# Kernel tuning notes

Measured on AMD Instinct MI355X. Metric: run time of the kernel, lower is better.

The kernel has to match this reference:

```python
import jax, jax.numpy as jnp
import numpy as np

NH, NKV, HD, H = 32, 8, 128, 4096
G = NH // NKV  # GQA group size = 4
EPS = 1e-5
SCALE = HD ** -0.5


def rms_norm(x, w, eps=EPS):
    # per-head RMSNorm over last dim, computed in fp32
    xf = x.astype(jnp.float32)
    var = jnp.mean(xf * xf, axis=-1, keepdims=True)
    return (w * (xf * jax.lax.rsqrt(var + eps)).astype(x.dtype))


def setup_inputs() -> dict:
    key = jax.random.key(0)
    ks = jax.random.split(key, 4)
    B, SQ, SKV = 4, 1024, 1601
    return {
        "hidden_states": jax.random.normal(ks[0], (B, SQ, H), jnp.float32),
        "cross_attention_states": jax.random.normal(ks[1], (B, SKV, H), jnp.float32),
        "wqkv": jax.random.normal(ks[2], ((NH + 2 * NKV) * HD, H), jnp.float32) * 0.02,
        "wo": jax.random.normal(ks[3], (NH * HD, H), jnp.float32) * 0.02,
        "q_norm_weight": jnp.ones((HD,), jnp.float32),
        "k_norm_weight": jnp.ones((HD,), jnp.float32),
    }


def reference(hidden_states, cross_attention_states, wqkv, wo, q_norm_weight, k_norm_weight):
    B, SQ, _ = hidden_states.shape
    SKV = cross_attention_states.shape[1]
    q_sz, kv_sz = NH * HD, NKV * HD

    # fused QKV projection on decoder tokens -> keep only q
    qkv_dec = jnp.einsum('bsh,oh->bso', hidden_states, wqkv)
    q = qkv_dec[..., :q_sz]
    # fused QKV projection on encoder tokens -> keep only k, v
    qkv_enc = jnp.einsum('bsh,oh->bso', cross_attention_states, wqkv)
    k = qkv_enc[..., q_sz:q_sz + kv_sz]
    v = qkv_enc[..., q_sz + kv_sz:]

    q = rms_norm(q.reshape(B, SQ, NH, HD), q_norm_weight)      # [B,SQ,NH,HD]
    k = rms_norm(k.reshape(B, SKV, NKV, HD), k_norm_weight)    # [B,SKV,NKV,HD]
    v = v.reshape(B, SKV, NKV, HD)

    # GQA: group query heads per kv head
    qg = q.reshape(B, SQ, NKV, G, HD)
    scores = jnp.einsum('bqkgd,bskd->bkgqs', qg, k) * SCALE    # [B,NKV,G,SQ,SKV]
    probs = jax.nn.softmax(scores, axis=-1)
    out = jnp.einsum('bkgqs,bskd->bqkgd', probs, v)            # [B,SQ,NKV,G,HD]
    out = out.reshape(B, SQ, NH * HD)
    return jnp.einsum('bso,ho->bsh', out, wo.T.T) if False else jnp.einsum('bsf,hf->bsh', out, wo)
```

## Files before the change

### kernel.cpp

```cpp
#include <hip/hip_runtime.h>
#include <cstdint>
#include <math.h>

typedef _Float16 f16;
typedef __attribute__((ext_vector_type(4))) _Float16 f16x4;
typedef __attribute__((ext_vector_type(8))) _Float16 f16x8;
typedef __attribute__((ext_vector_type(4))) float f32x4;

__device__ inline void gload_lds16(const void* g, void* l) {
  auto gp = reinterpret_cast<const __attribute__((address_space(1))) uint32_t*>(
      reinterpret_cast<uintptr_t>(g));
  auto lp = reinterpret_cast<__attribute__((address_space(3))) uint32_t*>(
      reinterpret_cast<uintptr_t>(l));
  __builtin_amdgcn_global_load_lds(gp, lp, 16 , 0, 0);
}

__global__ __launch_bounds__(256) void cvtzero_kernel(const float* __restrict__ s0, f16* __restrict__ d0,
                                                      const float* __restrict__ s1, f16* __restrict__ d1,
                                                      const float* __restrict__ s2, f16* __restrict__ d2,
                                                      float4* __restrict__ z) {
  int idx = blockIdx.x * blockDim.x + threadIdx.x;
  int stride = gridDim.x * blockDim.x;
  for (int i = idx; i < 18747392; i += stride) {
    const float* src; f16* dst; int k;
    if (i < 4194304) { src = s0; dst = d0; k = i; }
    else if (i < 10752000) { src = s1; dst = d1; k = i - 4194304; }
    else if (i < 17043456) { src = s2; dst = d2; k = i - 10752000; }
    else { float4 zr = {0.f, 0.f, 0.f, 0.f}; z[i - 17043456] = zr; continue; }
    float4 v = reinterpret_cast<const float4*>(src)[k];
    f16x4 h;
    h.x = (f16)v.x; h.y = (f16)v.y; h.z = (f16)v.z; h.w = (f16)v.w;
    reinterpret_cast<f16x4*>(dst)[k] = h;
  }
}

__global__ __launch_bounds__(256) void cvt_kernel(const float* __restrict__ src,
                                                  f16* __restrict__ dst, int n4) {
  int idx = blockIdx.x * blockDim.x + threadIdx.x;
  int stride = gridDim.x * blockDim.x;
  for (int i = idx; i < n4; i += stride) {
    float4 v = reinterpret_cast<const float4*>(src)[i];
    f16x4 h;
    h.x = (f16)v.x; h.y = (f16)v.y; h.z = (f16)v.z; h.w = (f16)v.w;
    reinterpret_cast<f16x4*>(dst)[i] = h;
  }
}

template <bool MB, int EPI>
__global__ __launch_bounds__(512, 2) void gemm256(const f16* __restrict__ A,
                                                  const f16* __restrict__ Bw,
                                                  float* __restrict__ C,
                                                  f16* __restrict__ Ch,
                                                  const float* __restrict__ wvec,
                                                  f16* __restrict__ Vtf,
                                                  int M, int N, int K) {
  __shared__ f16 As[2][256][64];
  __shared__ f16 Bs[2][256][64];
  const int tid = threadIdx.x;
  const int l = tid & 63, w = tid >> 6;
  const int lq = l & 15, lk = l >> 4;
  const int wm = w >> 2, wn = w & 3;
  const int nwg = gridDim.x * gridDim.y;
  const int p = blockIdx.y * gridDim.x + blockIdx.x;
  const int L = (p & 7) * (nwg >> 3) + (p >> 3);
  const int bx = L % gridDim.x, by = L / gridDim.x;
  const int brow = by * 256, bcol = bx * 256;
  const int KT = K >> 6;

  const int srow8 = w * 8 + (l >> 3);
  const int scol  = ((l & 7) ^ (l >> 3)) * 8;
  const int swz   = (lq & 7) << 4;

  f32x4 acc[8][4];
  f32x4 zf = {0.f, 0.f, 0.f, 0.f};
#pragma unroll
  for (int m = 0; m < 8; ++m)
#pragma unroll
    for (int n = 0; n < 4; ++n) acc[m][n] = zf;

  auto stageA = [&](int kt, int buf, int i) {
    int ra = brow + i * 64 + srow8;
    if (MB) ra = (ra < M) ? ra : (M - 1);
    gload_lds16(A + (size_t)ra * K + kt * 64 + scol,
                (char*)(&As[buf][0][0]) + i * 8192 + w * 1024);
  };
  auto stageB = [&](int kt, int buf, int i) {
    int rb = bcol + i * 64 + srow8;
    gload_lds16(Bw + (size_t)rb * K + kt * 64 + scol,
                (char*)(&Bs[buf][0][0]) + i * 8192 + w * 1024);
  };
  auto ldA = [&](int buf, int m, int kk) -> f16x8 {
    int r = wm * 128 + m * 16 + lq;
    return *reinterpret_cast<const f16x8*>(
        (char*)(&As[buf][0][0]) + r * 128 + ((kk * 64 + lk * 16) ^ swz));
  };
  auto ldB = [&](int buf, int n, int kk) -> f16x8 {
    int r = wn * 64 + n * 16 + lq;
    return *reinterpret_cast<const f16x8*>(
        (char*)(&Bs[buf][0][0]) + r * 128 + ((kk * 64 + lk * 16) ^ swz));
  };

#pragma unroll
  for (int i = 0; i < 4; ++i) stageA(0, 0, i);
#pragma unroll
  for (int i = 0; i < 4; ++i) stageB(0, 0, i);

  f16x8 avA[4][2], avB[4][2], bvA[2][2], bvB[2][2];
  for (int t = 0; t < KT; ++t) {
    const int buf = t & 1, nbuf = buf ^ 1;
    const bool pf = (t + 1 < KT);

    if (pf) {
      stageA(t + 1, nbuf, 0); stageA(t + 1, nbuf, 1);
      asm volatile("s_waitcnt vmcnt(2)" ::: "memory");
    } else {
      asm volatile("s_waitcnt vmcnt(0)" ::: "memory");
    }
    __builtin_amdgcn_s_barrier();

#pragma unroll
    for (int mm = 0; mm < 4; ++mm)
#pragma unroll
      for (int kk = 0; kk < 2; ++kk) avA[mm][kk] = ldA(buf, mm, kk);
#pragma unroll
    for (int nn = 0; nn < 2; ++nn)
#pragma unroll
      for (int kk = 0; kk < 2; ++kk) bvA[nn][kk] = ldB(buf, nn, kk);
    __builtin_amdgcn_s_setprio(1);
#pragma unroll
    for (int mm = 0; mm < 4; ++mm)
#pragma unroll
      for (int nn = 0; nn < 2; ++nn)
#pragma unroll
        for (int kk = 0; kk < 2; ++kk)
          acc[mm][nn] = __builtin_amdgcn_mfma_f32_16x16x32_f16(avA[mm][kk], bvA[nn][kk], acc[mm][nn], 0, 0, 0);
    __builtin_amdgcn_s_setprio(0);
#pragma unroll
    for (int mm = 0; mm < 4; ++mm)
#pragma unroll
      for (int kk = 0; kk < 2; ++kk) avB[mm][kk] = ldA(buf, 4 + mm, kk);
    if (pf) { stageA(t + 1, nbuf, 2); stageA(t + 1, nbuf, 3); }
    asm volatile("" ::: "memory");
    __builtin_amdgcn_s_barrier();

    __builtin_amdgcn_s_setprio(1);
#pragma unroll
    for (int mm = 0; mm < 4; ++mm)
#pragma unroll
      for (int nn = 0; nn < 2; ++nn)
#pragma unroll
        for (int kk = 0; kk < 2; ++kk)
          acc[4 + mm][nn] = __builtin_amdgcn_mfma_f32_16x16x32_f16(avB[mm][kk], bvA[nn][kk], acc[4 + mm][nn], 0, 0, 0);
    __builtin_amdgcn_s_setprio(0);
#pragma unroll
    for (int nn = 0; nn < 2; ++nn)
#pragma unroll
      for (int kk = 0; kk < 2; ++kk) bvB[nn][kk] = ldB(buf, 2 + nn, kk);
    if (pf) { stageB(t + 1, nbuf, 0); stageB(t + 1, nbuf, 1); }
    asm volatile("" ::: "memory");
    __builtin_amdgcn_s_barrier();

    __builtin_amdgcn_s_setprio(1);
#pragma unroll
    for (int mm = 0; mm < 4; ++mm)
#pragma unroll
      for (int nn = 0; nn < 2; ++nn)
#pragma unroll
        for (int kk = 0; kk < 2; ++kk)
          acc[4 + mm][2 + nn] = __builtin_amdgcn_mfma_f32_16x16x32_f16(avB[mm][kk], bvB[nn][kk], acc[4 + mm][2 + nn], 0, 0, 0);
    __builtin_amdgcn_s_setprio(0);
#pragma unroll
    for (int mm = 0; mm < 4; ++mm)
#pragma unroll
      for (int kk = 0; kk < 2; ++kk) avA[mm][kk] = ldA(buf, mm, kk);
    if (pf) { stageB(t + 1, nbuf, 2); stageB(t + 1, nbuf, 3); }
    asm volatile("" ::: "memory");
    __builtin_amdgcn_s_barrier();

    __builtin_amdgcn_s_setprio(1);
#pragma unroll
    for (int mm = 0; mm < 4; ++mm)
#pragma unroll
      for (int nn = 0; nn < 2; ++nn)
#pragma unroll
        for (int kk = 0; kk < 2; ++kk)
          acc[mm][2 + nn] = __builtin_amdgcn_mfma_f32_16x16x32_f16(avA[mm][kk], bvB[nn][kk], acc[mm][2 + nn], 0, 0, 0);
    __builtin_amdgcn_s_setprio(0);
  }

  if (EPI == 0) {
#pragma unroll
    for (int m = 0; m < 8; ++m) {
#pragma unroll
      for (int j = 0; j < 4; ++j) {
        int row = brow + wm * 128 + m * 16 + lk * 4 + j;
        if (MB && row >= M) continue;
        float* dst = C + (size_t)row * N + bcol + wn * 64 + lq;
#pragma unroll
        for (int n = 0; n < 4; ++n) dst[n * 16] = acc[m][n][j];
      }
    }
  } else if (EPI == 1) {
    __shared__ float ssq[256][4];
#pragma unroll
    for (int m = 0; m < 8; ++m)
#pragma unroll
      for (int j = 0; j < 4; ++j) {
        int lr = wm * 128 + m * 16 + lk * 4 + j;
        float pp = 0.f;
#pragma unroll
        for (int n = 0; n < 4; ++n) pp += acc[m][n][j] * acc[m][n][j];
        pp += __shfl_xor(pp, 1);
        pp += __shfl_xor(pp, 2);
        pp += __shfl_xor(pp, 4);
        pp += __shfl_xor(pp, 8);
        if (lq == 0) ssq[lr][wn] = pp;
      }
    asm volatile("" ::: "memory");
    __builtin_amdgcn_s_barrier();
    const int hh = wn >> 1;
    float wv[4];
#pragma unroll
    for (int n = 0; n < 4; ++n) wv[n] = wvec[(wn * 64 + n * 16 + lq) & 127];
#pragma unroll
    for (int m = 0; m < 8; ++m)
#pragma unroll
      for (int j = 0; j < 4; ++j) {
        int lr = wm * 128 + m * 16 + lk * 4 + j;
        float ss = ssq[lr][hh * 2] + ssq[lr][hh * 2 + 1];
        float rs = rsqrtf(ss * (1.0f / 128.0f) + 1e-5f) *
                   (0.08838834764831845f * 1.4426950408889634f);
        f16* dst = Ch + (size_t)(brow + lr) * N + bcol + wn * 64 + lq;
#pragma unroll
        for (int n = 0; n < 4; ++n) dst[n * 16] = (f16)(acc[m][n][j] * rs * wv[n]);
      }
  } else {
    const bool isK = (bcol < 1024);
    __shared__ float ssq[256][4];
    if (isK) {
#pragma unroll
      for (int m = 0; m < 8; ++m)
#pragma unroll
        for (int j = 0; j < 4; ++j) {
          int lr = wm * 128 + m * 16 + lk * 4 + j;
          float pp = 0.f;
#pragma unroll
          for (int n = 0; n < 4; ++n) pp += acc[m][n][j] * acc[m][n][j];
          pp += __shfl_xor(pp, 1);
          pp += __shfl_xor(pp, 2);
          pp += __shfl_xor(pp, 4);
          pp += __shfl_xor(pp, 8);
          if (lq == 0) ssq[lr][wn] = pp;
        }
      asm volatile("" ::: "memory");
      __builtin_amdgcn_s_barrier();
    }
    const int hh = wn >> 1;
    float wv[4];
    if (isK) {
#pragma unroll
      for (int n = 0; n < 4; ++n) wv[n] = wvec[(wn * 64 + n * 16 + lq) & 127];
    }
#pragma unroll
    for (int m = 0; m < 8; ++m) {
#pragma unroll
      for (int j = 0; j < 4; ++j) {
        int lr = wm * 128 + m * 16 + lk * 4 + j;
        int r = brow + lr;
        if (r >= M) continue;
        unsigned bb = (unsigned)r / 1601u;
        unsigned s = (unsigned)r - bb * 1601u;
        if (isK) {
          float ss = ssq[lr][hh * 2] + ssq[lr][hh * 2 + 1];
          float rs = rsqrtf(ss * (1.0f / 128.0f) + 1e-5f);
#pragma unroll
          for (int n = 0; n < 4; ++n) {
            int col = wn * 64 + n * 16 + lq;
            int kvh = (bcol + col) >> 7;
            int d = col & 127;
            Ch[((size_t)(bb * 8 + kvh) * 1664 + s) * 128 + d] =
                (f16)(acc[m][n][j] * rs * wv[n]);
          }
        } else {
#pragma unroll
          for (int n = 0; n < 4; ++n) {
            int col = bcol - 1024 + wn * 64 + n * 16 + lq;
            int kvh = col >> 7;
            int d = col & 127;
            Vtf[((size_t)(bb * 8 + kvh) * 128 + d) * 1664 + s] = (f16)acc[m][n][j];
          }
        }
      }
    }
  }
}

__global__ __launch_bounds__(512, 4) void attn_kernel(const f16* __restrict__ Qf,
                                                      const f16* __restrict__ Kf,
                                                      const f16* __restrict__ Vtf,
                                                      f16* __restrict__ Oa) {
  __shared__ f16 Ksm[2][64][128];
  __shared__ f16 Vsm[2][128][64];
  __shared__ f16 Psm[8][16][64];
  const int p = blockIdx.x;
  const int L = (p & 7) * 128 + (p >> 3);
  const int qt = L & 7, h = (L >> 3) & 31, b = L >> 8;
  const int kvh = h >> 2;
  const int tid = threadIdx.x;
  const int l = tid & 63, w = tid >> 6;
  const int lq = l & 15, lk = l >> 4;

  f16x8 qreg[4];
  const f16* Qbase = Qf + ((size_t)(b * 1024 + qt * 128 + w * 16)) * 4096 + h * 128;
#pragma unroll
  for (int ks = 0; ks < 4; ++ks)
    qreg[ks] = *reinterpret_cast<const f16x8*>(
        Qbase + (size_t)lq * 4096 + ks * 32 + lk * 8);

  const f16* Kb = Kf + (size_t)(b * 8 + kvh) * (1664 * 128);
  const f16* Vb = Vtf + (size_t)(b * 8 + kvh) * (128 * 1664);

  f32x4 o[8];
  f32x4 zf = {0.f, 0.f, 0.f, 0.f};
  f32x4 neg8 = {-8.f, -8.f, -8.f, -8.f};
#pragma unroll
  for (int dn = 0; dn < 8; ++dn) o[dn] = zf;
  float lrow[4];
#pragma unroll
  for (int j = 0; j < 4; ++j) lrow[j] = 0.f;

  char* Pw = (char*)(&Psm[w][0][0]);
  const int swzR = (lq & 7) << 4;

  auto stageK = [&](int t, int buf) {
#pragma unroll
    for (int i = 0; i < 2; ++i) {
      int row = w * 8 + i * 4 + lk;
      int cb = (lq * 16) ^ ((row & 7) << 4);
      gload_lds16(Kb + (size_t)(t * 64 + row) * 128 + (cb >> 1),
                  (char*)(&Ksm[buf][0][0]) + w * 2048 + i * 1024);
    }
  };
  auto stageV = [&](int t, int buf) {
#pragma unroll
    for (int i = 0; i < 2; ++i) {
      int r = w * 16 + i * 8 + (l >> 3);
      int cb = ((l & 7) * 16) ^ ((r & 7) << 4);
      gload_lds16(Vb + (size_t)r * 1664 + t * 64 + (cb >> 1),
                  (char*)(&Vsm[buf][0][0]) + w * 2048 + i * 1024);
    }
  };

  stageK(0, 0);
  stageV(0, 0);
  int cur = 0;
  for (int t = 0; t < 26; ++t) {
    if (t < 25) {
      stageK(t + 1, cur ^ 1);
      stageV(t + 1, cur ^ 1);
      asm volatile("s_waitcnt vmcnt(4)" ::: "memory");
    } else {
      asm volatile("s_waitcnt vmcnt(0)" ::: "memory");
    }
    __builtin_amdgcn_s_barrier();

    f32x4 s[4];
#pragma unroll
    for (int kn = 0; kn < 4; ++kn) s[kn] = neg8;
    __builtin_amdgcn_s_setprio(1);
#pragma unroll
    for (int ks = 0; ks < 4; ++ks) {
      f16x8 bf[4];
#pragma unroll
      for (int kn = 0; kn < 4; ++kn)
        bf[kn] = *reinterpret_cast<const f16x8*>(
            (char*)(&Ksm[cur][0][0]) + (kn * 16 + lq) * 256 + ((ks * 64 + lk * 16) ^ swzR));
#pragma unroll
      for (int kn = 0; kn < 4; ++kn)
        s[kn] = __builtin_amdgcn_mfma_f32_16x16x32_f16(qreg[ks], bf[kn], s[kn], 0, 0, 0);
    }
    __builtin_amdgcn_s_setprio(0);

    if (t == 25) {
#pragma unroll
      for (int kn = 0; kn < 4; ++kn) {
        bool valid = (kn * 16 + lq) < 1;
#pragma unroll
        for (int j = 0; j < 4; ++j) s[kn][j] = valid ? s[kn][j] : -1e30f;
      }
    }

#pragma unroll
    for (int j = 0; j < 4; ++j) {
      float rsum = 0.f;
#pragma unroll
      for (int kn = 0; kn < 4; ++kn) {
        float pv = exp2f(s[kn][j]);
        s[kn][j] = pv;
        rsum += pv;
      }
      lrow[j] += rsum;
      int prow = lk * 4 + j;
      int swzW = (prow & 7) << 4;
#pragma unroll
      for (int kn = 0; kn < 4; ++kn)
        *reinterpret_cast<f16*>(Pw + prow * 128 + (((kn * 16 + lq) * 2) ^ swzW)) =
            (f16)s[kn][j];
    }

    __builtin_amdgcn_s_setprio(1);
#pragma unroll
    for (int c = 0; c < 2; ++c) {
      f16x8 pa = *reinterpret_cast<const f16x8*>(
          Pw + lq * 128 + ((c * 64 + lk * 16) ^ swzR));
      f16x8 vb[8];
#pragma unroll
      for (int dn = 0; dn < 8; ++dn)
        vb[dn] = *reinterpret_cast<const f16x8*>(
            (char*)(&Vsm[cur][0][0]) + (dn * 16 + lq) * 128 + ((c * 64 + lk * 16) ^ swzR));
#pragma unroll
      for (int dn = 0; dn < 8; ++dn)
        o[dn] = __builtin_amdgcn_mfma_f32_16x16x32_f16(pa, vb[dn], o[dn], 0, 0, 0);
    }
    __builtin_amdgcn_s_setprio(0);
    __builtin_amdgcn_s_barrier();
    cur ^= 1;
  }

#pragma unroll
  for (int j = 0; j < 4; ++j) {
    float fl = lrow[j];
    fl += __shfl_xor(fl, 1);
    fl += __shfl_xor(fl, 2);
    fl += __shfl_xor(fl, 4);
    fl += __shfl_xor(fl, 8);
    float il = 1.0f / fl;
    int token = b * 1024 + qt * 128 + w * 16 + lk * 4 + j;
    f16* dst = Oa + (size_t)token * 4096 + h * 128;
#pragma unroll
    for (int dn = 0; dn < 8; ++dn) dst[dn * 16 + lq] = (f16)(o[dn][j] * il);
  }
}

extern "C" void kernel_launch(void* const* d_in, const int* in_sizes, int n_in,
                              void* d_out, int out_size, void* d_ws, size_t ws_size,
                              hipStream_t stream) {
  const float* hidden = (const float*)d_in[0];
  const float* cross  = (const float*)d_in[1];
  const float* wqkv   = (const float*)d_in[2];
  const float* wo     = (const float*)d_in[3];
  const float* qw     = (const float*)d_in[4];
  const float* kw     = (const float*)d_in[5];

  char* ws = (char*)d_ws;
  f16* hidden_h = (f16*)(ws + 0);
  f16* attn_h   = hidden_h;
  f16* wqkv_h = (f16*)(ws + 33554432);
  f16* cross_h = (f16*)(ws + 83886080);
  f16* wo_h    = (f16*)(ws + 83886080);
  f16* k_h  = (f16*)(ws + 136347648);
  f16* vt_h = (f16*)(ws + 136347648 + 13631488);
  f16* q_h = (f16*)d_out;

  cvtzero_kernel<<<2048, 256, 0, stream>>>(hidden, hidden_h, cross, cross_h,
                                           wqkv, wqkv_h, (float4*)(ws + 136347648));
  gemm256<true, 2><<<dim3(8, 26), 512, 0, stream>>>(
      cross_h, wqkv_h + (size_t)4096 * 4096, nullptr, k_h, kw, vt_h, 6404, 2048, 4096);
  cvt_kernel<<<2048, 256, 0, stream>>>(wo, wo_h, 16777216 / 4);
  gemm256<false, 1><<<dim3(16, 16), 512, 0, stream>>>(
      hidden_h, wqkv_h, nullptr, q_h, qw, nullptr, 4096, 4096, 4096);
  attn_kernel<<<1024, 512, 0, stream>>>(q_h, k_h, vt_h, attn_h);
  gemm256<false, 0><<<dim3(16, 16), 512, 0, stream>>>(
      attn_h, wo_h, (float*)d_out, nullptr, nullptr, nullptr, 4096, 4096, 4096);
}
```

Baseline: 613.5 us.

## Give each attention wave two query sub-tiles to reuse K/V LDS fragments

```diff
diff --git a/kernel.cpp b/kernel.cpp
--- a/kernel.cpp
+++ b/kernel.cpp
@@ -295,13 +295,13 @@
   }
 }
 
-__global__ __launch_bounds__(512, 4) void attn_kernel(const f16* __restrict__ Qf,
+__global__ __launch_bounds__(256, 2) void attn_kernel(const f16* __restrict__ Qf,
                                                       const f16* __restrict__ Kf,
                                                       const f16* __restrict__ Vtf,
                                                       f16* __restrict__ Oa) {
   __shared__ f16 Ksm[2][64][128];
   __shared__ f16 Vsm[2][128][64];
-  __shared__ f16 Psm[8][16][64];
+  __shared__ f16 Psm[4][32][64];
   const int p = blockIdx.x;
   const int L = (p & 7) * 128 + (p >> 3);
   const int qt = L & 7, h = (L >> 3) & 31, b = L >> 8;
@@ -310,44 +310,50 @@
   const int l = tid & 63, w = tid >> 6;
   const int lq = l & 15, lk = l >> 4;
 
-  f16x8 qreg[4];
-  const f16* Qbase = Qf + ((size_t)(b * 1024 + qt * 128 + w * 16)) * 4096 + h * 128;
-#pragma unroll
-  for (int ks = 0; ks < 4; ++ks)
-    qreg[ks] = *reinterpret_cast<const f16x8*>(
-        Qbase + (size_t)lq * 4096 + ks * 32 + lk * 8);
+  f16x8 qreg[2][4];
+  const f16* Qbase = Qf + ((size_t)(b * 1024 + qt * 128 + w * 32)) * 4096 + h * 128;
+#pragma unroll
+  for (int qm = 0; qm < 2; ++qm)
+#pragma unroll
+    for (int ks = 0; ks < 4; ++ks)
+      qreg[qm][ks] = *reinterpret_cast<const f16x8*>(
+          Qbase + (size_t)(qm * 16 + lq) * 4096 + ks * 32 + lk * 8);
 
   const f16* Kb = Kf + (size_t)(b * 8 + kvh) * (1664 * 128);
   const f16* Vb = Vtf + (size_t)(b * 8 + kvh) * (128 * 1664);
 
-  f32x4 o[8];
+  f32x4 o[2][8];
   f32x4 zf = {0.f, 0.f, 0.f, 0.f};
   f32x4 neg8 = {-8.f, -8.f, -8.f, -8.f};
 #pragma unroll
-  for (int dn = 0; dn < 8; ++dn) o[dn] = zf;
-  float lrow[4];
-#pragma unroll
-  for (int j = 0; j < 4; ++j) lrow[j] = 0.f;
+  for (int qm = 0; qm < 2; ++qm)
+#pragma unroll
+    for (int dn = 0; dn < 8; ++dn) o[qm][dn] = zf;
+  float lrow[2][4];
+#pragma unroll
+  for (int qm = 0; qm < 2; ++qm)
+#pragma unroll
+    for (int j = 0; j < 4; ++j) lrow[qm][j] = 0.f;
 
   char* Pw = (char*)(&Psm[w][0][0]);
   const int swzR = (lq & 7) << 4;
 
   auto stageK = [&](int t, int buf) {
 #pragma unroll
-    for (int i = 0; i < 2; ++i) {
-      int row = w * 8 + i * 4 + lk;
+    for (int i = 0; i < 4; ++i) {
+      int row = w * 16 + i * 4 + lk;
       int cb = (lq * 16) ^ ((row & 7) << 4);
       gload_lds16(Kb + (size_t)(t * 64 + row) * 128 + (cb >> 1),
-                  (char*)(&Ksm[buf][0][0]) + w * 2048 + i * 1024);
+                  (char*)(&Ksm[buf][0][0]) + w * 4096 + i * 1024);
     }
   };
   auto stageV = [&](int t, int buf) {
 #pragma unroll
-    for (int i = 0; i < 2; ++i) {
-      int r = w * 16 + i * 8 + (l >> 3);
+    for (int i = 0; i < 4; ++i) {
+      int r = w * 32 + i * 8 + (l >> 3);
       int cb = ((l & 7) * 16) ^ ((r & 7) << 4);
       gload_lds16(Vb + (size_t)r * 1664 + t * 64 + (cb >> 1),
-                  (char*)(&Vsm[buf][0][0]) + w * 2048 + i * 1024);
+                  (char*)(&Vsm[buf][0][0]) + w * 4096 + i * 1024);
     }
   };
 
@@ -358,15 +364,17 @@
     if (t < 25) {
       stageK(t + 1, cur ^ 1);
       stageV(t + 1, cur ^ 1);
-      asm volatile("s_waitcnt vmcnt(4)" ::: "memory");
+      asm volatile("s_waitcnt vmcnt(8)" ::: "memory");
     } else {
       asm volatile("s_waitcnt vmcnt(0)" ::: "memory");
     }
     __builtin_amdgcn_s_barrier();
 
-    f32x4 s[4];
-#pragma unroll
-    for (int kn = 0; kn < 4; ++kn) s[kn] = neg8;
+    f32x4 s[2][4];
+#pragma unroll
+    for (int qm = 0; qm < 2; ++qm)
+#pragma unroll
+      for (int kn = 0; kn < 4; ++kn) s[qm][kn] = neg8;
     __builtin_amdgcn_s_setprio(1);
 #pragma unroll
     for (int ks = 0; ks < 4; ++ks) {
@@ -376,8 +384,10 @@
         bf[kn] = *reinterpret_cast<const f16x8*>(
             (char*)(&Ksm[cur][0][0]) + (kn * 16 + lq) * 256 + ((ks * 64 + lk * 16) ^ swzR));
 #pragma unroll
-      for (int kn = 0; kn < 4; ++kn)
-        s[kn] = __builtin_amdgcn_mfma_f32_16x16x32_f16(qreg[ks], bf[kn], s[kn], 0, 0, 0);
+      for (int qm = 0; qm < 2; ++qm)
+#pragma unroll
+        for (int kn = 0; kn < 4; ++kn)
+          s[qm][kn] = __builtin_amdgcn_mfma_f32_16x16x32_f16(qreg[qm][ks], bf[kn], s[qm][kn], 0, 0, 0);
     }
     __builtin_amdgcn_s_setprio(0);
 
@@ -386,41 +396,53 @@
       for (int kn = 0; kn < 4; ++kn) {
         bool valid = (kn * 16 + lq) < 1;
 #pragma unroll
-        for (int j = 0; j < 4; ++j) s[kn][j] = valid ? s[kn][j] : -1e30f;
-      }
-    }
-
-#pragma unroll
-    for (int j = 0; j < 4; ++j) {
-      float rsum = 0.f;
-#pragma unroll
-      for (int kn = 0; kn < 4; ++kn) {
-        float pv = exp2f(s[kn][j]);
-        s[kn][j] = pv;
-        rsum += pv;
-      }
-      lrow[j] += rsum;
-      int prow = lk * 4 + j;
-      int swzW = (prow & 7) << 4;
-#pragma unroll
-      for (int kn = 0; kn < 4; ++kn)
-        *reinterpret_cast<f16*>(Pw + prow * 128 + (((kn * 16 + lq) * 2) ^ swzW)) =
-            (f16)s[kn][j];
+        for (int qm = 0; qm < 2; ++qm)
+#pragma unroll
+          for (int j = 0; j < 4; ++j) s[qm][kn][j] = valid ? s[qm][kn][j] : -1e30f;
+      }
+    }
+
+#pragma unroll
+    for (int qm = 0; qm < 2; ++qm) {
+#pragma unroll
+      for (int j = 0; j < 4; ++j) {
+        float rsum = 0.f;
+#pragma unroll
+        for (int kn = 0; kn < 4; ++kn) {
+          float pv = exp2f(s[qm][kn][j]);
+          s[qm][kn][j] = pv;
+          rsum += pv;
+        }
+        lrow[qm][j] += rsum;
+        int prow = qm * 16 + lk * 4 + j;
+        int swzW = lk << 5;
+#pragma unroll
+        for (int kn = 0; kn < 4; ++kn)
+          *reinterpret_cast<f16*>(Pw + prow * 128 + (((kn * 16 + lq) * 2) ^ swzW)) =
+              (f16)s[qm][kn][j];
+      }
     }
 
     __builtin_amdgcn_s_setprio(1);
 #pragma unroll
     for (int c = 0; c < 2; ++c) {
-      f16x8 pa = *reinterpret_cast<const f16x8*>(
-          Pw + lq * 128 + ((c * 64 + lk * 16) ^ swzR));
+      f16x8 pa[2];
+#pragma unroll
+      for (int qm = 0; qm < 2; ++qm) {
+        int prow = qm * 16 + lq;
+        pa[qm] = *reinterpret_cast<const f16x8*>(
+            Pw + prow * 128 + ((c * 64 + lk * 16) ^ (((lq >> 2) & 3) << 5)));
+      }
       f16x8 vb[8];
 #pragma unroll
       for (int dn = 0; dn < 8; ++dn)
         vb[dn] = *reinterpret_cast<const f16x8*>(
             (char*)(&Vsm[cur][0][0]) + (dn * 16 + lq) * 128 + ((c * 64 + lk * 16) ^ swzR));
 #pragma unroll
-      for (int dn = 0; dn < 8; ++dn)
-        o[dn] = __builtin_amdgcn_mfma_f32_16x16x32_f16(pa, vb[dn], o[dn], 0, 0, 0);
+      for (int qm = 0; qm < 2; ++qm)
+#pragma unroll
+        for (int dn = 0; dn < 8; ++dn)
+          o[qm][dn] = __builtin_amdgcn_mfma_f32_16x16x32_f16(pa[qm], vb[dn], o[qm][dn], 0, 0, 0);
     }
     __builtin_amdgcn_s_setprio(0);
     __builtin_amdgcn_s_barrier();
@@ -428,17 +450,20 @@
   }
 
 #pragma unroll
-  for (int j = 0; j < 4; ++j) {
-    float fl = lrow[j];
-    fl += __shfl_xor(fl, 1);
-    fl += __shfl_xor(fl, 2);
-    fl += __shfl_xor(fl, 4);
-    fl += __shfl_xor(fl, 8);
-    float il = 1.0f / fl;
-    int token = b * 1024 + qt * 128 + w * 16 + lk * 4 + j;
-    f16* dst = Oa + (size_t)token * 4096 + h * 128;
-#pragma unroll
-    for (int dn = 0; dn < 8; ++dn) dst[dn * 16 + lq] = (f16)(o[dn][j] * il);
+  for (int qm = 0; qm < 2; ++qm) {
+#pragma unroll
+    for (int j = 0; j < 4; ++j) {
+      float fl = lrow[qm][j];
+      fl += __shfl_xor(fl, 1);
+      fl += __shfl_xor(fl, 2);
+      fl += __shfl_xor(fl, 4);
+      fl += __shfl_xor(fl, 8);
+      float il = 1.0f / fl;
+      int token = b * 1024 + qt * 128 + w * 32 + qm * 16 + lk * 4 + j;
+      f16* dst = Oa + (size_t)token * 4096 + h * 128;
+#pragma unroll
+      for (int dn = 0; dn < 8; ++dn) dst[dn * 16 + lq] = (f16)(o[qm][dn][j] * il);
+    }
   }
 }
 
@@ -469,7 +494,7 @@
   cvt_kernel<<<2048, 256, 0, stream>>>(wo, wo_h, 16777216 / 4);
   gemm256<false, 1><<<dim3(16, 16), 512, 0, stream>>>(
       hidden_h, wqkv_h, nullptr, q_h, qw, nullptr, 4096, 4096, 4096);
-  attn_kernel<<<1024, 512, 0, stream>>>(q_h, k_h, vt_h, attn_h);
+  attn_kernel<<<1024, 256, 0, stream>>>(q_h, k_h, vt_h, attn_h);
   gemm256<false, 0><<<dim3(16, 16), 512, 0, stream>>>(
       attn_h, wo_h, (float*)d_out, nullptr, nullptr, nullptr, 4096, 4096, 4096);
 }
```

Measured after the change: 605.7 us. About the same (-1.3%).
